# Performance work log

Hardware: AMD Instinct MI355X
Metric: run time of the kernel (lower is better)

Reference implementation:

```python
import jax, jax.numpy as jnp
import numpy as np

N, C, HS, D, B = 50000, 64, 64, 128, 512

def setup_inputs() -> dict:
    key = jax.random.key(0)
    ks = jax.random.split(key, 10)
    return {
        "x": jax.random.normal(ks[0], (N, D), jnp.float32),
        "pos": jax.random.normal(ks[1], (N, 3), jnp.float32),
        "batch": jax.random.randint(ks[2], (N,), 0, B, jnp.int64),
        "centers": jax.random.normal(ks[3], (C, 3), jnp.float32),
        "widths": jnp.ones((C,), jnp.float32),
        "W1": jax.random.normal(ks[4], (D, HS), jnp.float32) * (1.0 / np.sqrt(D)),
        "b1": jnp.zeros((HS,), jnp.float32),
        "Wa": jax.random.normal(ks[5], (HS, 1), jnp.float32) * (1.0 / np.sqrt(HS)),
        "ba": jnp.zeros((1,), jnp.float32),
        "W2": jax.random.normal(ks[6], (HS, D), jnp.float32) * (1.0 / np.sqrt(HS)),
        "b2": jnp.zeros((D,), jnp.float32),
        "gamma": jnp.ones((D,), jnp.float32),
        "beta": jnp.zeros((D,), jnp.float32),
        "W3": jax.random.normal(ks[7], (D, 1), jnp.float32) * (1.0 / np.sqrt(D)),
        "b3": jnp.zeros((1,), jnp.float32),
    }

def reference(x, pos, batch, centers, widths, W1, b1, Wa, ba, W2, b2, gamma, beta, W3, b3):
    # per-node hidden features [N, HS]
    x1 = x @ W1 + b1
    # gaussian RBF: exp(-||pos - c|| / width^2)  -> [N, C]
    dist = jnp.sqrt(jnp.sum((pos[:, None, :] - centers[None, :, :]) ** 2, axis=2))
    rbf = jnp.exp(-dist / (widths ** 2))
    # outer product [N, C, HS] then scatter-add by graph id -> [B, C, HS]
    mul = rbf[:, :, None] * x1[:, None, :]
    feat = jax.ops.segment_sum(mul, batch, num_segments=B)
    # attention over the C centers
    w = feat @ Wa + ba                      # [B, C, 1]
    attn = jax.nn.softmax(w, axis=1)
    agg = jnp.sum(attn * feat, axis=1)      # [B, HS]
    # MLP head: LeakyReLU(0.2) -> LayerNorm -> Linear to scalar
    h = agg @ W2 + b2                       # [B, D]
    h = jnp.where(h >= 0, h, 0.2 * h)
    mu = jnp.mean(h, axis=-1, keepdims=True)
    var = jnp.mean((h - mu) ** 2, axis=-1, keepdims=True)
    h = (h - mu) * jax.lax.rsqrt(var + 1e-5) * gamma + beta
    return h @ W3 + b3                      # [B, 1]
```

## Files before the change

### kernel.cpp

```cpp
#include <hip/hip_runtime.h>


__global__ __launch_bounds__(256) void hist_k(const int* __restrict__ batch, int n, int* __restrict__ cnt) {
    for (int i = blockIdx.x * blockDim.x + threadIdx.x; i < n; i += gridDim.x * blockDim.x)
        atomicAdd(&cnt[batch[i]], 1);
}

__global__ __launch_bounds__(512) void scan_k(const int* __restrict__ cnt, int* __restrict__ offs,
                                              int* __restrict__ cursor) {
    __shared__ int s[512];
    int t = threadIdx.x;
    s[t] = cnt[t];
    __syncthreads();
    for (int o = 1; o < 512; o <<= 1) {
        int v = (t >= o) ? s[t - o] : 0;
        __syncthreads();
        s[t] += v;
        __syncthreads();
    }
    offs[t + 1] = s[t];
    if (t == 0) offs[0] = 0;
    cursor[t] = s[t] - cnt[t];
}

__global__ __launch_bounds__(256) void scatter_k(const int* __restrict__ batch, int n,
                                                 int* __restrict__ cursor, int* __restrict__ order) {
    for (int i = blockIdx.x * blockDim.x + threadIdx.x; i < n; i += gridDim.x * blockDim.x) {
        int p = atomicAdd(&cursor[batch[i]], 1);
        order[p] = i;
    }
}

__global__ __launch_bounds__(256) void fused_k(
    const float* __restrict__ x, const float* __restrict__ pos,
    const int* __restrict__ order, const int* __restrict__ offs,
    const float* __restrict__ centers, const float* __restrict__ widths,
    const float* __restrict__ W1, const float* __restrict__ b1,
    const float* __restrict__ Wa, const float* __restrict__ ba,
    const float* __restrict__ W2, const float* __restrict__ b2,
    const float* __restrict__ gamma_, const float* __restrict__ beta_,
    const float* __restrict__ W3, const float* __restrict__ b3,
    float* __restrict__ out)
{
    __shared__ float W1s[128][64];
    __shared__ float cxs[64], cys[64], czs[64], iw2[64], Was[64], b1s[64];
    __shared__ float xs[4][128];
    __shared__ float ps[4][3];
    __shared__ float part[4][4][64];
    __shared__ float x1s[4][64];
    __shared__ float rbfs[4][64];
    __shared__ float feats[64][65];
    __shared__ float wred[8];
    __shared__ float attn[64], aggs[64];

    const int t = threadIdx.x;
    const int b = blockIdx.x;
    const int h = t & 63;
    const int q = t >> 6;

    for (int k = t; k < 128 * 64; k += 256) W1s[k >> 6][k & 63] = W1[k];
    if (t < 64) {
        cxs[t] = centers[3 * t]; cys[t] = centers[3 * t + 1]; czs[t] = centers[3 * t + 2];
        float w = widths[t];
        iw2[t] = 1.0f / (w * w);
        Was[t] = Wa[t];
        b1s[t] = b1[t];
    }
    float acc[16];
    #pragma unroll
    for (int k = 0; k < 16; ++k) acc[k] = 0.f;

    const int start = offs[b], end = offs[b + 1];
    __syncthreads();

    for (int base = start; base < end; base += 4) {
        const int nn = min(4, end - base);
        for (int k = t; k < nn * 128; k += 256) {
            int n = k >> 7, d = k & 127;
            xs[n][d] = x[(size_t)order[base + n] * 128 + d];
        }
        if (t < nn * 3) {
            int n = t / 3, c = t % 3;
            ps[n][c] = pos[(size_t)order[base + n] * 3 + c];
        }
        __syncthreads();
        for (int n = 0; n < nn; ++n) {
            float s = 0.f;
            #pragma unroll
            for (int d = 0; d < 32; ++d) s += xs[n][q * 32 + d] * W1s[q * 32 + d][h];
            part[n][q][h] = s;
        }
        __syncthreads();
        if (q < nn) {
            x1s[q][h] = part[q][0][h] + part[q][1][h] + part[q][2][h] + part[q][3][h] + b1s[h];
            float dx = ps[q][0] - cxs[h], dy = ps[q][1] - cys[h], dz = ps[q][2] - czs[h];
            float dist = sqrtf(dx * dx + dy * dy + dz * dz);
            rbfs[q][h] = __expf(-dist * iw2[h]);
        }
        __syncthreads();
        for (int n = 0; n < nn; ++n) {
            float xv = x1s[n][h];
            #pragma unroll
            for (int k = 0; k < 16; ++k) acc[k] += rbfs[n][q * 16 + k] * xv;
        }
        __syncthreads();
    }

    #pragma unroll
    for (int k = 0; k < 16; ++k) feats[q * 16 + k][h] = acc[k];
    __syncthreads();

    if (t < 64) {
        float s = 0.f;
        #pragma unroll
        for (int hh = 0; hh < 64; ++hh) s += feats[t][hh] * Was[hh];
        s += ba[0];
        float m = s;
        #pragma unroll
        for (int o = 32; o > 0; o >>= 1) m = fmaxf(m, __shfl_xor(m, o, 64));
        float e = __expf(s - m);
        float se = e;
        #pragma unroll
        for (int o = 32; o > 0; o >>= 1) se += __shfl_xor(se, o, 64);
        attn[t] = e / se;
    }
    __syncthreads();
    if (t < 64) {
        float s = 0.f;
        #pragma unroll
        for (int c = 0; c < 64; ++c) s += attn[c] * feats[c][t];
        aggs[t] = s;
    }
    __syncthreads();

    float hv = 0.f;
    if (t < 128) {
        float s = 0.f;
        #pragma unroll
        for (int hh = 0; hh < 64; ++hh) s += aggs[hh] * W2[hh * 128 + t];
        s += b2[t];
        hv = (s >= 0.f) ? s : 0.2f * s;
    }
    float r = hv;
    #pragma unroll
    for (int o = 32; o > 0; o >>= 1) r += __shfl_xor(r, o, 64);
    if ((t & 63) == 0) wred[t >> 6] = r;
    __syncthreads();
    float mu = (wred[0] + wred[1]) * (1.f / 128.f);
    float dv = (t < 128) ? (hv - mu) : 0.f;
    r = dv * dv;
    #pragma unroll
    for (int o = 32; o > 0; o >>= 1) r += __shfl_xor(r, o, 64);
    __syncthreads();
    if ((t & 63) == 0) wred[t >> 6] = r;
    __syncthreads();
    float var = (wred[0] + wred[1]) * (1.f / 128.f);
    float rstd = rsqrtf(var + 1e-5f);
    float p = 0.f;
    if (t < 128) {
        float nv = (hv - mu) * rstd * gamma_[t] + beta_[t];
        p = nv * W3[t];
    }
    r = p;
    #pragma unroll
    for (int o = 32; o > 0; o >>= 1) r += __shfl_xor(r, o, 64);
    __syncthreads();
    if ((t & 63) == 0) wred[t >> 6] = r;
    __syncthreads();
    if (t == 0) out[b] = wred[0] + wred[1] + b3[0];
}

extern "C" void kernel_launch(void* const* d_in, const int* in_sizes, int n_in,
                              void* d_out, int out_size, void* d_ws, size_t ws_size,
                              hipStream_t stream) {
    const float* x       = (const float*)d_in[0];
    const float* pos     = (const float*)d_in[1];
    const int*   batch   = (const int*)d_in[2];
    const float* centers = (const float*)d_in[3];
    const float* widths  = (const float*)d_in[4];
    const float* W1      = (const float*)d_in[5];
    const float* b1      = (const float*)d_in[6];
    const float* Wa      = (const float*)d_in[7];
    const float* ba      = (const float*)d_in[8];
    const float* W2      = (const float*)d_in[9];
    const float* b2      = (const float*)d_in[10];
    const float* gamma_  = (const float*)d_in[11];
    const float* beta_   = (const float*)d_in[12];
    const float* W3      = (const float*)d_in[13];
    const float* b3      = (const float*)d_in[14];
    float* out = (float*)d_out;

    const int N = in_sizes[1] / 3;
    const int B = out_size;

    int* wsI    = (int*)d_ws;
    int* cnt    = wsI;
    int* offs   = wsI + 512;
    int* cursor = wsI + 1026;
    int* order  = wsI + 1540;

    hipMemsetAsync(cnt, 0, 512 * sizeof(int), stream);
    int blocks = (N + 255) / 256;
    hist_k<<<blocks, 256, 0, stream>>>(batch, N, cnt);
    scan_k<<<1, 512, 0, stream>>>(cnt, offs, cursor);
    scatter_k<<<blocks, 256, 0, stream>>>(batch, N, cursor, order);
    fused_k<<<B, 256, 0, stream>>>(x, pos, order, offs, centers, widths,
                                   W1, b1, Wa, ba, W2, b2, gamma_, beta_, W3, b3, out);
}
```

Baseline: 126.3 us.

## Split per-graph kernel into node-tiled accumulation with atomics plus separate head

The single per-graph kernel is replaced by two kernels. The first processes fixed 64-node tiles of the sorted order, using W1 held in registers and float4 loads, and flushes per-graph partial feature sums to a global buffer with atomicAdd whenever the graph id changes. The second runs the attention and MLP head per graph from that buffer. This is meant to fix load imbalance and underuse of the GPU with only 512 blocks and 4-node steps. The cost is an 8 MB memset, atomic traffic, and a global round trip for the features.

```diff
diff --git a/kernel.cpp b/kernel.cpp
--- a/kernel.cpp
+++ b/kernel.cpp
@@ -31,89 +31,131 @@
     }
 }
 
-__global__ __launch_bounds__(256) void fused_k(
+__global__ __launch_bounds__(256) void featacc_k(
     const float* __restrict__ x, const float* __restrict__ pos,
-    const int* __restrict__ order, const int* __restrict__ offs,
+    const int* __restrict__ batch, const int* __restrict__ order,
     const float* __restrict__ centers, const float* __restrict__ widths,
     const float* __restrict__ W1, const float* __restrict__ b1,
+    float* __restrict__ feats_g, int N)
+{
+    constexpr int TILE = 64, SUB = 16;
+    __shared__ float xs[SUB][128];
+    __shared__ float part[SUB][4][64];
+    __shared__ float x1s[SUB][64];
+    __shared__ float rbfs[SUB][64];
+    __shared__ float ps[SUB][3];
+    __shared__ int   bids[TILE];
+    __shared__ int   ords[TILE];
+
+    const int t = threadIdx.x;
+    const int h = t & 63;
+    const int q = t >> 6;
+    const int base = blockIdx.x * TILE;
+    const int cnt = min(TILE, N - base);
+
+    float w1r[32];
+    #pragma unroll
+    for (int d = 0; d < 32; ++d) w1r[d] = W1[(size_t)(32 * q + d) * 64 + h];
+
+    const float cx = centers[3 * h], cy = centers[3 * h + 1], cz = centers[3 * h + 2];
+    const float w  = widths[h];
+    const float iw2v = 1.0f / (w * w);
+    const float b1v  = b1[h];
+
+    if (t < cnt) { int o = order[base + t]; ords[t] = o; bids[t] = batch[o]; }
+    __syncthreads();
+
+    float acc[16];
+    #pragma unroll
+    for (int k = 0; k < 16; ++k) acc[k] = 0.f;
+    int cur_b = bids[0];
+
+    for (int sb = 0; sb < cnt; sb += SUB) {
+        const int nn = min(SUB, cnt - sb);
+        for (int k = t; k < nn * 32; k += 256) {
+            int n = k >> 5, d4 = k & 31;
+            ((float4*)xs[n])[d4] = ((const float4*)(x + (size_t)ords[sb + n] * 128))[d4];
+        }
+        if (t < nn * 3) { int n = t / 3, c = t % 3; ps[n][c] = pos[(size_t)ords[sb + n] * 3 + c]; }
+        __syncthreads();
+
+        for (int n = 0; n < nn; ++n) {
+            const float4* xr = (const float4*)&xs[n][32 * q];
+            float s = 0.f;
+            #pragma unroll
+            for (int d4 = 0; d4 < 8; ++d4) {
+                float4 v = xr[d4];
+                s += v.x * w1r[4 * d4] + v.y * w1r[4 * d4 + 1]
+                   + v.z * w1r[4 * d4 + 2] + v.w * w1r[4 * d4 + 3];
+            }
+            part[n][q][h] = s;
+        }
+        __syncthreads();
+
+        #pragma unroll
+        for (int j = 0; j < 4; ++j) {
+            int n = q * 4 + j;
+            if (n < nn) {
+                x1s[n][h] = part[n][0][h] + part[n][1][h] + part[n][2][h] + part[n][3][h] + b1v;
+                float dx = ps[n][0] - cx, dy = ps[n][1] - cy, dz = ps[n][2] - cz;
+                rbfs[n][h] = __expf(-sqrtf(dx * dx + dy * dy + dz * dz) * iw2v);
+            }
+        }
+        __syncthreads();
+
+        for (int n = 0; n < nn; ++n) {
+            int bb = bids[sb + n];
+            if (bb != cur_b) {
+                float* fg = feats_g + ((size_t)cur_b * 64 + q * 16) * 64 + h;
+                #pragma unroll
+                for (int k = 0; k < 16; ++k) { atomicAdd(fg + (size_t)k * 64, acc[k]); acc[k] = 0.f; }
+                cur_b = bb;
+            }
+            float xv = x1s[n][h];
+            const float4* rr = (const float4*)&rbfs[n][16 * q];
+            #pragma unroll
+            for (int k4 = 0; k4 < 4; ++k4) {
+                float4 rv = rr[k4];
+                acc[4 * k4 + 0] += rv.x * xv;
+                acc[4 * k4 + 1] += rv.y * xv;
+                acc[4 * k4 + 2] += rv.z * xv;
+                acc[4 * k4 + 3] += rv.w * xv;
+            }
+        }
+        __syncthreads();
+    }
+    float* fg = feats_g + ((size_t)cur_b * 64 + q * 16) * 64 + h;
+    #pragma unroll
+    for (int k = 0; k < 16; ++k) atomicAdd(fg + (size_t)k * 64, acc[k]);
+}
+
+__global__ __launch_bounds__(128) void head_k(
+    const float* __restrict__ feats_g,
     const float* __restrict__ Wa, const float* __restrict__ ba,
     const float* __restrict__ W2, const float* __restrict__ b2,
     const float* __restrict__ gamma_, const float* __restrict__ beta_,
     const float* __restrict__ W3, const float* __restrict__ b3,
     float* __restrict__ out)
 {
-    __shared__ float W1s[128][64];
-    __shared__ float cxs[64], cys[64], czs[64], iw2[64], Was[64], b1s[64];
-    __shared__ float xs[4][128];
-    __shared__ float ps[4][3];
-    __shared__ float part[4][4][64];
-    __shared__ float x1s[4][64];
-    __shared__ float rbfs[4][64];
-    __shared__ float feats[64][65];
-    __shared__ float wred[8];
-    __shared__ float attn[64], aggs[64];
-
+    __shared__ float fbs[64][65];
+    __shared__ float attn_s[64];
+    __shared__ float aggs[64];
+    __shared__ float red[2];
     const int t = threadIdx.x;
     const int b = blockIdx.x;
-    const int h = t & 63;
-    const int q = t >> 6;
-
-    for (int k = t; k < 128 * 64; k += 256) W1s[k >> 6][k & 63] = W1[k];
-    if (t < 64) {
-        cxs[t] = centers[3 * t]; cys[t] = centers[3 * t + 1]; czs[t] = centers[3 * t + 2];
-        float w = widths[t];
-        iw2[t] = 1.0f / (w * w);
-        Was[t] = Wa[t];
-        b1s[t] = b1[t];
-    }
-    float acc[16];
-    #pragma unroll
-    for (int k = 0; k < 16; ++k) acc[k] = 0.f;
-
-    const int start = offs[b], end = offs[b + 1];
-    __syncthreads();
-
-    for (int base = start; base < end; base += 4) {
-        const int nn = min(4, end - base);
-        for (int k = t; k < nn * 128; k += 256) {
-            int n = k >> 7, d = k & 127;
-            xs[n][d] = x[(size_t)order[base + n] * 128 + d];
-        }
-        if (t < nn * 3) {
-            int n = t / 3, c = t % 3;
-            ps[n][c] = pos[(size_t)order[base + n] * 3 + c];
-        }
-        __syncthreads();
-        for (int n = 0; n < nn; ++n) {
-            float s = 0.f;
-            #pragma unroll
-            for (int d = 0; d < 32; ++d) s += xs[n][q * 32 + d] * W1s[q * 32 + d][h];
-            part[n][q][h] = s;
-        }
-        __syncthreads();
-        if (q < nn) {
-            x1s[q][h] = part[q][0][h] + part[q][1][h] + part[q][2][h] + part[q][3][h] + b1s[h];
-            float dx = ps[q][0] - cxs[h], dy = ps[q][1] - cys[h], dz = ps[q][2] - czs[h];
-            float dist = sqrtf(dx * dx + dy * dy + dz * dz);
-            rbfs[q][h] = __expf(-dist * iw2[h]);
-        }
-        __syncthreads();
-        for (int n = 0; n < nn; ++n) {
-            float xv = x1s[n][h];
-            #pragma unroll
-            for (int k = 0; k < 16; ++k) acc[k] += rbfs[n][q * 16 + k] * xv;
-        }
-        __syncthreads();
-    }
-
-    #pragma unroll
-    for (int k = 0; k < 16; ++k) feats[q * 16 + k][h] = acc[k];
+    const float* fb = feats_g + (size_t)b * 4096;
+
+    for (int k = t; k < 1024; k += 128) {
+        float4 v = ((const float4*)fb)[k];
+        int c = k >> 4, d4 = (k & 15) * 4;
+        fbs[c][d4] = v.x; fbs[c][d4 + 1] = v.y; fbs[c][d4 + 2] = v.z; fbs[c][d4 + 3] = v.w;
+    }
     __syncthreads();
 
     if (t < 64) {
         float s = 0.f;
         #pragma unroll
-        for (int hh = 0; hh < 64; ++hh) s += feats[t][hh] * Was[hh];
+        for (int hh = 0; hh < 64; ++hh) s += fbs[t][hh] * Wa[hh];
         s += ba[0];
         float m = s;
         #pragma unroll
@@ -122,52 +164,45 @@
         float se = e;
         #pragma unroll
         for (int o = 32; o > 0; o >>= 1) se += __shfl_xor(se, o, 64);
-        attn[t] = e / se;
+        attn_s[t] = e / se;
     }
     __syncthreads();
     if (t < 64) {
         float s = 0.f;
         #pragma unroll
-        for (int c = 0; c < 64; ++c) s += attn[c] * feats[c][t];
+        for (int c = 0; c < 64; ++c) s += attn_s[c] * fbs[c][t];
         aggs[t] = s;
     }
     __syncthreads();
 
-    float hv = 0.f;
-    if (t < 128) {
-        float s = 0.f;
-        #pragma unroll
-        for (int hh = 0; hh < 64; ++hh) s += aggs[hh] * W2[hh * 128 + t];
-        s += b2[t];
-        hv = (s >= 0.f) ? s : 0.2f * s;
-    }
+    float s = 0.f;
+    #pragma unroll
+    for (int hh = 0; hh < 64; ++hh) s += aggs[hh] * W2[hh * 128 + t];
+    s += b2[t];
+    float hv = (s >= 0.f) ? s : 0.2f * s;
+
     float r = hv;
     #pragma unroll
     for (int o = 32; o > 0; o >>= 1) r += __shfl_xor(r, o, 64);
-    if ((t & 63) == 0) wred[t >> 6] = r;
-    __syncthreads();
-    float mu = (wred[0] + wred[1]) * (1.f / 128.f);
-    float dv = (t < 128) ? (hv - mu) : 0.f;
+    if ((t & 63) == 0) red[t >> 6] = r;
+    __syncthreads();
+    float mu = (red[0] + red[1]) * (1.f / 128.f);
+    float dv = hv - mu;
     r = dv * dv;
     #pragma unroll
     for (int o = 32; o > 0; o >>= 1) r += __shfl_xor(r, o, 64);
     __syncthreads();
-    if ((t & 63) == 0) wred[t >> 6] = r;
-    __syncthreads();
-    float var = (wred[0] + wred[1]) * (1.f / 128.f);
-    float rstd = rsqrtf(var + 1e-5f);
-    float p = 0.f;
-    if (t < 128) {
-        float nv = (hv - mu) * rstd * gamma_[t] + beta_[t];
-        p = nv * W3[t];
-    }
-    r = p;
+    if ((t & 63) == 0) red[t >> 6] = r;
+    __syncthreads();
+    float var = (red[0] + red[1]) * (1.f / 128.f);
+    float nv = dv * rsqrtf(var + 1e-5f) * gamma_[t] + beta_[t];
+    r = nv * W3[t];
     #pragma unroll
     for (int o = 32; o > 0; o >>= 1) r += __shfl_xor(r, o, 64);
     __syncthreads();
-    if ((t & 63) == 0) wred[t >> 6] = r;
-    __syncthreads();
-    if (t == 0) out[b] = wred[0] + wred[1] + b3[0];
+    if ((t & 63) == 0) red[t >> 6] = r;
+    __syncthreads();
+    if (t == 0) out[b] = red[0] + red[1] + b3[0];
 }
 
 extern "C" void kernel_launch(void* const* d_in, const int* in_sizes, int n_in,
@@ -193,17 +228,20 @@
     const int N = in_sizes[1] / 3;
     const int B = out_size;
 
-    int* wsI    = (int*)d_ws;
-    int* cnt    = wsI;
-    int* offs   = wsI + 512;
-    int* cursor = wsI + 1026;
-    int* order  = wsI + 1540;
-
-    hipMemsetAsync(cnt, 0, 512 * sizeof(int), stream);
+    int*   wsI     = (int*)d_ws;
+    int*   cnt     = wsI;
+    int*   offs    = wsI + 512;
+    int*   cursor  = wsI + 1026;
+    float* feats_g = (float*)(wsI + 1540);
+    int*   order   = wsI + 1540 + 512 * 4096;
+
+    hipMemsetAsync(wsI, 0, (size_t)(1540 + 512 * 4096) * sizeof(int), stream);
+
     int blocks = (N + 255) / 256;
     hist_k<<<blocks, 256, 0, stream>>>(batch, N, cnt);
     scan_k<<<1, 512, 0, stream>>>(cnt, offs, cursor);
     scatter_k<<<blocks, 256, 0, stream>>>(batch, N, cursor, order);
-    fused_k<<<B, 256, 0, stream>>>(x, pos, order, offs, centers, widths,
-                                   W1, b1, Wa, ba, W2, b2, gamma_, beta_, W3, b3, out);
-}
+    featacc_k<<<(N + 63) / 64, 256, 0, stream>>>(x, pos, batch, order, centers, widths,
+                                                 W1, b1, feats_g, N);
+    head_k<<<B, 128, 0, stream>>>(feats_g, Wa, ba, W2, b2, gamma_, beta_, W3, b3, out);
+}
```

After: 118.2 us. 1.07x faster.
